# Optimization experiments

Measured on AMD Instinct MI355X. Metric: run time of the kernel, lower is better.

Reference implementation:

```python
import jax, jax.numpy as jnp
import numpy as np

# model constants (match init_kwargs)
B, T, D = 2, 2048, 2048          # batch, seq_len, d_model (= d_in = d_out)
H, G = 32, 8                     # num_heads, num_kv_groups
HD = D // H                      # head_dim = 64
GROUP = H // G                   # 4 query heads per KV group
ROPE_BASE = 10000.0


def _apply_rope(x):
    # x: (b, heads, t, hd); rotate-half RoPE over absolute positions 0..t-1
    t = x.shape[2]
    half = HD // 2
    inv_freq = 1.0 / (ROPE_BASE ** (jnp.arange(half, dtype=jnp.float32) * 2.0 / HD))
    ang = jnp.arange(t, dtype=jnp.float32)[:, None] * inv_freq[None, :]   # (t, half)
    cos, sin = jnp.cos(ang), jnp.sin(ang)
    x1, x2 = x[..., :half], x[..., half:]
    out = jnp.concatenate([x1 * cos - x2 * sin, x2 * cos + x1 * sin], axis=-1)
    return out.astype(x.dtype)


def setup_inputs() -> dict:
    key = jax.random.key(0)
    kx, kq, kk, kv, ko = jax.random.split(key, 5)
    scale = 0.02
    x = jax.random.normal(kx, (B, T, D), dtype=jnp.float32)
    # linear weights stored as (in, out) so y = x @ W
    Wq = jax.random.normal(kq, (D, D), dtype=jnp.float32) * scale
    Wk = jax.random.normal(kk, (D, G * HD), dtype=jnp.float32) * scale
    Wv = jax.random.normal(kv, (D, G * HD), dtype=jnp.float32) * scale
    Wo = jax.random.normal(ko, (D, D), dtype=jnp.float32) * scale
    return {"x": x, "Wq": Wq, "Wk": Wk, "Wv": Wv, "Wo": Wo}


def reference(x, Wq, Wk, Wv, Wo):
    b, t, _ = x.shape
    q = (x @ Wq).reshape(b, t, H, HD).transpose(0, 2, 1, 3)   # (b, H, t, hd)
    k = (x @ Wk).reshape(b, t, G, HD).transpose(0, 2, 1, 3)   # (b, G, t, hd)
    v = (x @ Wv).reshape(b, t, G, HD).transpose(0, 2, 1, 3)
    q = _apply_rope(q)
    k = _apply_rope(k)
    # GQA: physically duplicate K/V per query-head group (repeat_interleave)
    k = jnp.repeat(k, GROUP, axis=1)                          # (b, H, t, hd)
    v = jnp.repeat(v, GROUP, axis=1)
    scores = jnp.einsum('bhqd,bhkd->bhqk', q, k)              # (b, H, t, t)
    causal = jnp.triu(jnp.ones((t, t), dtype=bool), k=1)
    scores = jnp.where(causal, -jnp.inf, scores)
    attn = jax.nn.softmax(scores / jnp.sqrt(jnp.float32(HD)), axis=-1)
    ctx = jnp.einsum('bhqk,bhkd->bhqd', attn, v)              # (b, H, t, hd)
    # faithful to source: transpose(-2, -1) then reshape (NOT the usual (b,t,H,hd) order)
    ctx = jnp.swapaxes(ctx, -2, -1).reshape(b, t, D)
    return ctx @ Wo
```

## Files before the change

kernel.cpp:

```cpp
#include <hip/hip_runtime.h>

typedef unsigned short u16;
typedef unsigned int u32;
typedef __bf16 bf16x8 __attribute__((ext_vector_type(8)));
typedef float f32x4 __attribute__((ext_vector_type(4)));
typedef u16 u16x8 __attribute__((ext_vector_type(8)));
typedef __attribute__((address_space(1))) const void gvoid;
typedef __attribute__((address_space(3))) void svoid;

#define T_SEQ 2048
#define NEG_INF (-__builtin_huge_valf())

__device__ __forceinline__ u16 f2bf(float f) {
  union { float f; unsigned u; } x; x.f = f;
  unsigned u = x.u;
  return (u16)((u + 0x7FFFu + ((u >> 16) & 1u)) >> 16);
}
__device__ __forceinline__ float bf2f(u16 h) {
  union { unsigned u; float f; } x; x.u = ((unsigned)h) << 16;
  return x.f;
}
__device__ __forceinline__ u32 pack_bf2(float lo, float hi) {
  u32 r;
  asm("v_cvt_pk_bf16_f32 %0, %1, %2" : "=v"(r) : "v"(lo), "v"(hi));
  return r;
}
__device__ __forceinline__ int swz16(int row, int col16) {
  int blk = (col16 >> 3) ^ (row & 7) ^ ((row >> 3) & 7);
  return row * 64 + ((blk & 7) << 3) + (col16 & 7);
}

__global__ __launch_bounds__(256) void cast_f32_bf16(const float* __restrict__ in,
                                                     u16* __restrict__ out, long n) {
  long i = ((long)blockIdx.x * 256 + threadIdx.x) * 4;
  if (i >= n) return;
  float4 v = *(const float4*)(in + i);
  ushort4 o;
  o.x = f2bf(v.x); o.y = f2bf(v.y); o.z = f2bf(v.z); o.w = f2bf(v.w);
  *(ushort4*)(out + i) = o;
}

__global__ __launch_bounds__(256) void transpose_cast(const float* __restrict__ W,
                                                      u16* __restrict__ WT, int K, int N) {
  __shared__ float tile[32][33];
  int nb = blockIdx.x * 32, kb = blockIdx.y * 32;
  int tx = threadIdx.x, ty = threadIdx.y;
  #pragma unroll
  for (int i = 0; i < 32; i += 8)
    tile[ty + i][tx] = W[(size_t)(kb + ty + i) * N + nb + tx];
  __syncthreads();
  #pragma unroll
  for (int i = 0; i < 32; i += 8)
    WT[(size_t)(nb + ty + i) * K + kb + tx] = f2bf(tile[tx][ty + i]);
}

__global__ __launch_bounds__(256) void rope_table_k(float2* __restrict__ tab) {
  int idx = blockIdx.x * 256 + threadIdx.x;
  int t = idx >> 5, d = idx & 31;
  float inv = powf(10000.0f, -(float)d / 32.0f);
  float ang = (float)t * inv;
  float s, c;
  sincosf(ang, &s, &c);
  tab[idx] = make_float2(c, s);
}

template<int MODE>
__global__ __launch_bounds__(256) void gemm_bt(const u16* __restrict__ A,
                                               const u16* __restrict__ BT,
                                               void* __restrict__ Cout,
                                               int M, int N, int K,
                                               const float2* __restrict__ tab) {
  __shared__ __align__(16) u16 As[128 * 64];
  __shared__ __align__(16) u16 Bs[128 * 64];
  const int tid = threadIdx.x;
  const int w = tid >> 6, lane = tid & 63;
  const int r16 = lane & 15, kg = lane >> 4;
  const size_t rowBase = (size_t)blockIdx.y * 128;
  const size_t colBase = (size_t)blockIdx.x * 128;
  const int wm = (w >> 1) * 64, wn = (w & 1) * 64;
  f32x4 acc[4][4] = {};

  const u16* Abase = A + (rowBase + w * 32 + (lane >> 3)) * (size_t)K + (lane & 7) * 8;
  const u16* Bbase = BT + (colBase + w * 32 + (lane >> 3)) * (size_t)K + (lane & 7) * 8;

  for (int k0 = 0; k0 < K; k0 += 64) {
    __syncthreads();
    #pragma unroll
    for (int i = 0; i < 4; ++i) {
      __builtin_amdgcn_global_load_lds((gvoid*)(Abase + (size_t)i * 8 * K + k0),
                                       (svoid*)(&As[(w * 32 + i * 8) * 64]), 16, 0, 0);
      __builtin_amdgcn_global_load_lds((gvoid*)(Bbase + (size_t)i * 8 * K + k0),
                                       (svoid*)(&Bs[(w * 32 + i * 8) * 64]), 16, 0, 0);
    }
    __syncthreads();
    #pragma unroll
    for (int kk = 0; kk < 2; ++kk) {
      bf16x8 af[4], bfv[4];
      #pragma unroll
      for (int mi = 0; mi < 4; ++mi)
        af[mi] = *(const bf16x8*)(&As[(wm + mi * 16 + r16) * 64 + kk * 32 + kg * 8]);
      #pragma unroll
      for (int ni = 0; ni < 4; ++ni)
        bfv[ni] = *(const bf16x8*)(&Bs[(wn + ni * 16 + r16) * 64 + kk * 32 + kg * 8]);
      __builtin_amdgcn_s_setprio(1);
      #pragma unroll
      for (int mi = 0; mi < 4; ++mi)
        #pragma unroll
        for (int ni = 0; ni < 4; ++ni)
          acc[mi][ni] = __builtin_amdgcn_mfma_f32_16x16x32_bf16(af[mi], bfv[ni], acc[mi][ni], 0, 0, 0);
      __builtin_amdgcn_s_setprio(0);
    }
  }

  if (MODE == 2 && colBase < 2560) {
    #pragma unroll
    for (int mi = 0; mi < 4; ++mi)
      #pragma unroll
      for (int p = 0; p < 2; ++p) {
        int d = (wn + p * 16 + r16) & 63;
        #pragma unroll
        for (int r = 0; r < 4; ++r) {
          int t = (int)((rowBase + wm + mi * 16 + kg * 4 + r) & (T_SEQ - 1));
          float2 cs = tab[t * 32 + d];
          float x1 = acc[mi][p][r], x2 = acc[mi][p + 2][r];
          acc[mi][p][r]     = x1 * cs.x - x2 * cs.y;
          acc[mi][p + 2][r] = x2 * cs.x + x1 * cs.y;
        }
      }
  }

  #pragma unroll
  for (int mi = 0; mi < 4; ++mi)
    #pragma unroll
    for (int ni = 0; ni < 4; ++ni) {
      size_t row = rowBase + wm + mi * 16 + kg * 4;
      size_t col = colBase + wn + ni * 16 + r16;
      if (MODE == 1) {
        float* C = (float*)Cout;
        #pragma unroll
        for (int r = 0; r < 4; ++r) C[(row + r) * N + col] = acc[mi][ni][r];
      } else {
        u16* C = (u16*)Cout;
        #pragma unroll
        for (int r = 0; r < 4; ++r) C[(row + r) * N + col] = f2bf(acc[mi][ni][r]);
      }
    }
}

__global__ __launch_bounds__(256) void attn_fwd(const u16* __restrict__ QKV,
                                                u16* __restrict__ ctxT) {
  const int bh = blockIdx.x, pr = blockIdx.y;
  const int b = bh >> 5, h = bh & 31, g = h >> 2;
  const int tid = threadIdx.x, w = tid >> 6, lane = tid & 63;
  const int r16 = lane & 15, kg = lane >> 4;
  const int LD = 3072;

  const u16* Qp = QKV + (size_t)b * T_SEQ * LD + h * 64;
  const u16* Kp = QKV + (size_t)b * T_SEQ * LD + 2048 + g * 64;
  const u16* Vp = QKV + (size_t)b * T_SEQ * LD + 2560 + g * 64;

  __shared__ __align__(16) u16 Kt[2][64 * 64];
  __shared__ __align__(16) u16 Vt[2][64 * 64];

  const float SCALE = 0.18033688f;
  const int srow = tid >> 3, sc8 = tid & 7;
  const int klr = (lane >> 3);
  const int kblk = lane & 7;

  for (int hf = 0; hf < 2; ++hf) {
    const int qt = hf ? (15 - pr) : pr;
    const int qbase = qt * 128, wq = qbase + w * 32;

    bf16x8 qf[2][2];
    #pragma unroll
    for (int mi = 0; mi < 2; ++mi)
      #pragma unroll
      for (int ks = 0; ks < 2; ++ks)
        qf[mi][ks] = *(const bf16x8*)(Qp + (size_t)(wq + mi * 16 + r16) * LD + ks * 32 + kg * 8);

    f32x4 acc[4][2] = {};
    float m_i[2] = {NEG_INF, NEG_INF}, l_i[2] = {0.0f, 0.0f};
    const int nkt = (qbase + 128) >> 6;

    {
      #pragma unroll
      for (int i = 0; i < 2; ++i) {
        int lr = w * 16 + i * 8 + klr;
        int sb = kblk ^ ((lr & 7) ^ ((lr >> 3) & 7));
        __builtin_amdgcn_global_load_lds((gvoid*)(Kp + (size_t)lr * LD + sb * 8),
                                         (svoid*)(&Kt[0][(w * 16 + i * 8) * 64]), 16, 0, 0);
      }
      bf16x8 v0 = *(const bf16x8*)(Vp + (size_t)(2 * srow) * LD + sc8 * 8);
      bf16x8 v1 = *(const bf16x8*)(Vp + (size_t)(2 * srow + 1) * LD + sc8 * 8);
      const u16* va = (const u16*)&v0;
      const u16* vb = (const u16*)&v1;
      #pragma unroll
      for (int j = 0; j < 8; ++j)
        *(u32*)(&Vt[0][swz16(sc8 * 8 + j, 2 * srow)]) = (u32)va[j] | ((u32)vb[j] << 16);
      __syncthreads();
    }

    for (int kt = 0; kt < nkt; ++kt) {
      const int kvb = kt << 6;
      const int cur = kt & 1;
      const bool st = (kt + 1 < nkt);
      bf16x8 v0, v1;
      if (st) {
        #pragma unroll
        for (int i = 0; i < 2; ++i) {
          int lr = w * 16 + i * 8 + klr;
          int sb = kblk ^ ((lr & 7) ^ ((lr >> 3) & 7));
          __builtin_amdgcn_global_load_lds((gvoid*)(Kp + (size_t)(kvb + 64 + lr) * LD + sb * 8),
                                           (svoid*)(&Kt[cur ^ 1][(w * 16 + i * 8) * 64]), 16, 0, 0);
        }
        v0 = *(const bf16x8*)(Vp + (size_t)(kvb + 64 + 2 * srow) * LD + sc8 * 8);
        v1 = *(const bf16x8*)(Vp + (size_t)(kvb + 64 + 2 * srow + 1) * LD + sc8 * 8);
      }

      if (kvb <= wq + 31) {
        f32x4 stv[4][2] = {};
        #pragma unroll
        for (int ks = 0; ks < 2; ++ks) {
          bf16x8 kf[4];
          #pragma unroll
          for (int ni = 0; ni < 4; ++ni)
            kf[ni] = *(const bf16x8*)(&Kt[cur][swz16(ni * 16 + r16, ks * 32 + kg * 8)]);
          __builtin_amdgcn_s_setprio(1);
          #pragma unroll
          for (int ni = 0; ni < 4; ++ni)
            #pragma unroll
            for (int mi = 0; mi < 2; ++mi)
              stv[ni][mi] = __builtin_amdgcn_mfma_f32_16x16x32_bf16(kf[ni], qf[mi][ks], stv[ni][mi], 0, 0, 0);
          __builtin_amdgcn_s_setprio(0);
        }

        if (kvb + 63 > wq) {
          #pragma unroll
          for (int mi = 0; mi < 2; ++mi) {
            const int q = wq + mi * 16 + r16;
            #pragma unroll
            for (int ni = 0; ni < 4; ++ni)
              #pragma unroll
              for (int r = 0; r < 4; ++r) {
                int kv = kvb + ni * 16 + kg * 4 + r;
                if (kv > q) stv[ni][mi][r] = NEG_INF;
              }
          }
        }

        float tmx[2];
        #pragma unroll
        for (int mi = 0; mi < 2; ++mi) {
          float pm = NEG_INF;
          #pragma unroll
          for (int ni = 0; ni < 4; ++ni)
            #pragma unroll
            for (int r = 0; r < 4; ++r) pm = fmaxf(pm, stv[ni][mi][r]);
          pm = fmaxf(pm, __shfl_xor(pm, 16, 64));
          pm = fmaxf(pm, __shfl_xor(pm, 32, 64));
          tmx[mi] = pm;
        }
        bool upd = ((tmx[0] - m_i[0]) * SCALE > 8.0f) || ((tmx[1] - m_i[1]) * SCALE > 8.0f);
        if (__any(upd)) {
          #pragma unroll
          for (int mi = 0; mi < 2; ++mi) {
            float mnew = fmaxf(m_i[mi], tmx[mi]);
            float alpha = exp2f((m_i[mi] - mnew) * SCALE);
            m_i[mi] = mnew;
            l_i[mi] *= alpha;
            #pragma unroll
            for (int di = 0; di < 4; ++di)
              #pragma unroll
              for (int r = 0; r < 4; ++r) acc[di][mi][r] *= alpha;
          }
        }

        u32 pkk[2][4][2];
        #pragma unroll
        for (int mi = 0; mi < 2; ++mi) {
          float nm = m_i[mi] * SCALE;
          float rs = 0.0f;
          #pragma unroll
          for (int ni = 0; ni < 4; ++ni) {
            float p0 = exp2f(fmaf(stv[ni][mi][0], SCALE, -nm));
            float p1 = exp2f(fmaf(stv[ni][mi][1], SCALE, -nm));
            float p2 = exp2f(fmaf(stv[ni][mi][2], SCALE, -nm));
            float p3 = exp2f(fmaf(stv[ni][mi][3], SCALE, -nm));
            rs += (p0 + p1) + (p2 + p3);
            pkk[mi][ni][0] = pack_bf2(p0, p1);
            pkk[mi][ni][1] = pack_bf2(p2, p3);
          }
          rs += __shfl_xor(rs, 16, 64);
          rs += __shfl_xor(rs, 32, 64);
          l_i[mi] += rs;
        }

        #pragma unroll
        for (int ks = 0; ks < 2; ++ks) {
          bf16x8 vfr[4];
          #pragma unroll
          for (int di = 0; di < 4; ++di)
            vfr[di] = *(const bf16x8*)(&Vt[cur][swz16(di * 16 + r16, ks * 32 + kg * 8)]);
          const int s0 = (kg & 1) * 32 + r16;
          const int s1 = s0 + 16;
          const bool hi = (kg >> 1) != 0;
          #pragma unroll
          for (int mi = 0; mi < 2; ++mi) {
            u32 a0 = __shfl(pkk[mi][2 * ks][0], s0, 64);
            u32 b0 = __shfl(pkk[mi][2 * ks + 1][0], s0, 64);
            u32 a1 = __shfl(pkk[mi][2 * ks][1], s0, 64);
            u32 b1 = __shfl(pkk[mi][2 * ks + 1][1], s0, 64);
            u32 a2 = __shfl(pkk[mi][2 * ks][0], s1, 64);
            u32 b2 = __shfl(pkk[mi][2 * ks + 1][0], s1, 64);
            u32 a3 = __shfl(pkk[mi][2 * ks][1], s1, 64);
            u32 b3 = __shfl(pkk[mi][2 * ks + 1][1], s1, 64);
            union { u32 u[4]; bf16x8 v; } pu;
            pu.u[0] = hi ? b0 : a0;
            pu.u[1] = hi ? b1 : a1;
            pu.u[2] = hi ? b2 : a2;
            pu.u[3] = hi ? b3 : a3;
            __builtin_amdgcn_s_setprio(1);
            #pragma unroll
            for (int di = 0; di < 4; ++di)
              acc[di][mi] = __builtin_amdgcn_mfma_f32_16x16x32_bf16(vfr[di], pu.v, acc[di][mi], 0, 0, 0);
            __builtin_amdgcn_s_setprio(0);
          }
        }
      }

      if (st) {
        const u16* va = (const u16*)&v0;
        const u16* vb = (const u16*)&v1;
        #pragma unroll
        for (int j = 0; j < 8; ++j)
          *(u32*)(&Vt[cur ^ 1][swz16(sc8 * 8 + j, 2 * srow)]) = (u32)va[j] | ((u32)vb[j] << 16);
      }
      __syncthreads();
    }

    float inv[2] = {1.0f / l_i[0], 1.0f / l_i[1]};
    #pragma unroll
    for (int di = 0; di < 4; ++di)
      #pragma unroll
      for (int mi = 0; mi < 2; ++mi)
        #pragma unroll
        for (int r = 0; r < 4; ++r) {
          size_t row = (size_t)(b * 2048 + h * 64 + di * 16 + kg * 4 + r);
          ctxT[row * 2048 + wq + mi * 16 + r16] = f2bf(acc[di][mi][r] * inv[mi]);
        }
  }
}

extern "C" void kernel_launch(void* const* d_in, const int* in_sizes, int n_in,
                              void* d_out, int out_size, void* d_ws, size_t ws_size,
                              hipStream_t stream) {
  const float* x  = (const float*)d_in[0];
  const float* Wq = (const float*)d_in[1];
  const float* Wk = (const float*)d_in[2];
  const float* Wv = (const float*)d_in[3];
  const float* Wo = (const float*)d_in[4];
  float* out = (float*)d_out;
  char* ws = (char*)d_ws;

  u16* xb     = (u16*)(ws);
  u16* QKVb   = (u16*)(ws + 16777216);
  u16* ctxT   = (u16*)(ws + 41943040);
  u16* WqkvT  = (u16*)(ws + 58720256);
  u16* WoT    = (u16*)(ws + 71303168);
  float2* tab = (float2*)(ws + 79691776);

  cast_f32_bf16<<<8192, 256, 0, stream>>>(x, xb, 8388608L);
  rope_table_k<<<256, 256, 0, stream>>>(tab);
  transpose_cast<<<dim3(64, 64), dim3(32, 8), 0, stream>>>(Wq, WqkvT, 2048, 2048);
  transpose_cast<<<dim3(16, 64), dim3(32, 8), 0, stream>>>(Wk, WqkvT + 2048L * 2048, 2048, 512);
  transpose_cast<<<dim3(16, 64), dim3(32, 8), 0, stream>>>(Wv, WqkvT + 2560L * 2048, 2048, 512);
  transpose_cast<<<dim3(64, 64), dim3(32, 8), 0, stream>>>(Wo, WoT, 2048, 2048);

  gemm_bt<2><<<dim3(24, 32), 256, 0, stream>>>(xb, WqkvT, QKVb, 4096, 3072, 2048, tab);

  attn_fwd<<<dim3(64, 8), 256, 0, stream>>>(QKVb, ctxT);

  gemm_bt<1><<<dim3(16, 32), 256, 0, stream>>>(ctxT, WoT, out, 4096, 2048, 2048, nullptr);
}
```

Measured before the change: 434.8 us.

## Split attention work across eight waves with 16 query rows each

```diff
diff --git a/kernel.cpp b/kernel.cpp
--- a/kernel.cpp
+++ b/kernel.cpp
@@ -4,7 +4,7 @@
 typedef unsigned int u32;
 typedef __bf16 bf16x8 __attribute__((ext_vector_type(8)));
 typedef float f32x4 __attribute__((ext_vector_type(4)));
-typedef u16 u16x8 __attribute__((ext_vector_type(8)));
+typedef u16 u16x4 __attribute__((ext_vector_type(4)));
 typedef __attribute__((address_space(1))) const void gvoid;
 typedef __attribute__((address_space(3))) void svoid;
 
@@ -15,10 +15,6 @@
   union { float f; unsigned u; } x; x.f = f;
   unsigned u = x.u;
   return (u16)((u + 0x7FFFu + ((u >> 16) & 1u)) >> 16);
-}
-__device__ __forceinline__ float bf2f(u16 h) {
-  union { unsigned u; float f; } x; x.u = ((unsigned)h) << 16;
-  return x.f;
 }
 __device__ __forceinline__ u32 pack_bf2(float lo, float hi) {
   u32 r;
@@ -147,8 +143,8 @@
     }
 }
 
-__global__ __launch_bounds__(256) void attn_fwd(const u16* __restrict__ QKV,
-                                                u16* __restrict__ ctxT) {
+__global__ __launch_bounds__(512, 4) void attn_fwd(const u16* __restrict__ QKV,
+                                                   u16* __restrict__ ctxT) {
   const int bh = blockIdx.x, pr = blockIdx.y;
   const int b = bh >> 5, h = bh & 31, g = h >> 2;
   const int tid = threadIdx.x, w = tid >> 6, lane = tid & 63;
@@ -163,40 +159,31 @@
   __shared__ __align__(16) u16 Vt[2][64 * 64];
 
   const float SCALE = 0.18033688f;
-  const int srow = tid >> 3, sc8 = tid & 7;
-  const int klr = (lane >> 3);
-  const int kblk = lane & 7;
+  const int srow = tid >> 4, sc4 = tid & 15;
+  const int klr = w * 8 + (lane >> 3);
+  const int ksb = (lane & 7) ^ (klr & 7) ^ ((klr >> 3) & 7);
 
   for (int hf = 0; hf < 2; ++hf) {
     const int qt = hf ? (15 - pr) : pr;
-    const int qbase = qt * 128, wq = qbase + w * 32;
-
-    bf16x8 qf[2][2];
-    #pragma unroll
-    for (int mi = 0; mi < 2; ++mi)
-      #pragma unroll
-      for (int ks = 0; ks < 2; ++ks)
-        qf[mi][ks] = *(const bf16x8*)(Qp + (size_t)(wq + mi * 16 + r16) * LD + ks * 32 + kg * 8);
-
-    f32x4 acc[4][2] = {};
-    float m_i[2] = {NEG_INF, NEG_INF}, l_i[2] = {0.0f, 0.0f};
-    const int nkt = (qbase + 128) >> 6;
+    const int qbase = qt * 128, wq = qbase + w * 16;
+    const int nkt = 2 * qt + 2;
+
+    bf16x8 qf[2];
+    #pragma unroll
+    for (int ks = 0; ks < 2; ++ks)
+      qf[ks] = *(const bf16x8*)(Qp + (size_t)(wq + r16) * LD + ks * 32 + kg * 8);
+
+    f32x4 acc[4] = {};
+    float m_i = NEG_INF, l_i = 0.0f;
 
     {
-      #pragma unroll
-      for (int i = 0; i < 2; ++i) {
-        int lr = w * 16 + i * 8 + klr;
-        int sb = kblk ^ ((lr & 7) ^ ((lr >> 3) & 7));
-        __builtin_amdgcn_global_load_lds((gvoid*)(Kp + (size_t)lr * LD + sb * 8),
-                                         (svoid*)(&Kt[0][(w * 16 + i * 8) * 64]), 16, 0, 0);
-      }
-      bf16x8 v0 = *(const bf16x8*)(Vp + (size_t)(2 * srow) * LD + sc8 * 8);
-      bf16x8 v1 = *(const bf16x8*)(Vp + (size_t)(2 * srow + 1) * LD + sc8 * 8);
-      const u16* va = (const u16*)&v0;
-      const u16* vb = (const u16*)&v1;
-      #pragma unroll
-      for (int j = 0; j < 8; ++j)
-        *(u32*)(&Vt[0][swz16(sc8 * 8 + j, 2 * srow)]) = (u32)va[j] | ((u32)vb[j] << 16);
+      __builtin_amdgcn_global_load_lds((gvoid*)(Kp + (size_t)klr * LD + ksb * 8),
+                                       (svoid*)(&Kt[0][w * 512]), 16, 0, 0);
+      u16x4 a0 = *(const u16x4*)(Vp + (size_t)(2 * srow) * LD + sc4 * 4);
+      u16x4 a1 = *(const u16x4*)(Vp + (size_t)(2 * srow + 1) * LD + sc4 * 4);
+      #pragma unroll
+      for (int j = 0; j < 4; ++j)
+        *(u32*)(&Vt[0][swz16(sc4 * 4 + j, 2 * srow)]) = (u32)a0[j] | ((u32)a1[j] << 16);
       __syncthreads();
     }
 
@@ -204,21 +191,16 @@
       const int kvb = kt << 6;
       const int cur = kt & 1;
       const bool st = (kt + 1 < nkt);
-      bf16x8 v0, v1;
+      u16x4 a0, a1;
       if (st) {
-        #pragma unroll
-        for (int i = 0; i < 2; ++i) {
-          int lr = w * 16 + i * 8 + klr;
-          int sb = kblk ^ ((lr & 7) ^ ((lr >> 3) & 7));
-          __builtin_amdgcn_global_load_lds((gvoid*)(Kp + (size_t)(kvb + 64 + lr) * LD + sb * 8),
-                                           (svoid*)(&Kt[cur ^ 1][(w * 16 + i * 8) * 64]), 16, 0, 0);
-        }
-        v0 = *(const bf16x8*)(Vp + (size_t)(kvb + 64 + 2 * srow) * LD + sc8 * 8);
-        v1 = *(const bf16x8*)(Vp + (size_t)(kvb + 64 + 2 * srow + 1) * LD + sc8 * 8);
-      }
-
-      if (kvb <= wq + 31) {
-        f32x4 stv[4][2] = {};
+        __builtin_amdgcn_global_load_lds((gvoid*)(Kp + (size_t)(kvb + 64 + klr) * LD + ksb * 8),
+                                         (svoid*)(&Kt[cur ^ 1][w * 512]), 16, 0, 0);
+        a0 = *(const u16x4*)(Vp + (size_t)(kvb + 64 + 2 * srow) * LD + sc4 * 4);
+        a1 = *(const u16x4*)(Vp + (size_t)(kvb + 64 + 2 * srow + 1) * LD + sc4 * 4);
+      }
+
+      if (kvb <= wq + 15) {
+        f32x4 stv[4] = {};
         #pragma unroll
         for (int ks = 0; ks < 2; ++ks) {
           bf16x8 kf[4];
@@ -228,72 +210,53 @@
           __builtin_amdgcn_s_setprio(1);
           #pragma unroll
           for (int ni = 0; ni < 4; ++ni)
-            #pragma unroll
-            for (int mi = 0; mi < 2; ++mi)
-              stv[ni][mi] = __builtin_amdgcn_mfma_f32_16x16x32_bf16(kf[ni], qf[mi][ks], stv[ni][mi], 0, 0, 0);
+            stv[ni] = __builtin_amdgcn_mfma_f32_16x16x32_bf16(kf[ni], qf[ks], stv[ni], 0, 0, 0);
           __builtin_amdgcn_s_setprio(0);
         }
 
         if (kvb + 63 > wq) {
-          #pragma unroll
-          for (int mi = 0; mi < 2; ++mi) {
-            const int q = wq + mi * 16 + r16;
-            #pragma unroll
-            for (int ni = 0; ni < 4; ++ni)
-              #pragma unroll
-              for (int r = 0; r < 4; ++r) {
-                int kv = kvb + ni * 16 + kg * 4 + r;
-                if (kv > q) stv[ni][mi][r] = NEG_INF;
-              }
-          }
-        }
-
-        float tmx[2];
-        #pragma unroll
-        for (int mi = 0; mi < 2; ++mi) {
-          float pm = NEG_INF;
+          const int q = wq + r16;
           #pragma unroll
           for (int ni = 0; ni < 4; ++ni)
             #pragma unroll
-            for (int r = 0; r < 4; ++r) pm = fmaxf(pm, stv[ni][mi][r]);
-          pm = fmaxf(pm, __shfl_xor(pm, 16, 64));
-          pm = fmaxf(pm, __shfl_xor(pm, 32, 64));
-          tmx[mi] = pm;
-        }
-        bool upd = ((tmx[0] - m_i[0]) * SCALE > 8.0f) || ((tmx[1] - m_i[1]) * SCALE > 8.0f);
-        if (__any(upd)) {
-          #pragma unroll
-          for (int mi = 0; mi < 2; ++mi) {
-            float mnew = fmaxf(m_i[mi], tmx[mi]);
-            float alpha = exp2f((m_i[mi] - mnew) * SCALE);
-            m_i[mi] = mnew;
-            l_i[mi] *= alpha;
+            for (int r = 0; r < 4; ++r)
+              if (kvb + ni * 16 + kg * 4 + r > q) stv[ni][r] = NEG_INF;
+        }
+
+        float pm = NEG_INF;
+        #pragma unroll
+        for (int ni = 0; ni < 4; ++ni)
+          #pragma unroll
+          for (int r = 0; r < 4; ++r) pm = fmaxf(pm, stv[ni][r]);
+        pm = fmaxf(pm, __shfl_xor(pm, 16, 64));
+        pm = fmaxf(pm, __shfl_xor(pm, 32, 64));
+        if (__any((pm - m_i) * SCALE > 8.0f)) {
+          float mnew = fmaxf(m_i, pm);
+          float alpha = exp2f((m_i - mnew) * SCALE);
+          m_i = mnew;
+          l_i *= alpha;
+          #pragma unroll
+          for (int di = 0; di < 4; ++di)
             #pragma unroll
-            for (int di = 0; di < 4; ++di)
-              #pragma unroll
-              for (int r = 0; r < 4; ++r) acc[di][mi][r] *= alpha;
-          }
-        }
-
-        u32 pkk[2][4][2];
-        #pragma unroll
-        for (int mi = 0; mi < 2; ++mi) {
-          float nm = m_i[mi] * SCALE;
-          float rs = 0.0f;
-          #pragma unroll
-          for (int ni = 0; ni < 4; ++ni) {
-            float p0 = exp2f(fmaf(stv[ni][mi][0], SCALE, -nm));
-            float p1 = exp2f(fmaf(stv[ni][mi][1], SCALE, -nm));
-            float p2 = exp2f(fmaf(stv[ni][mi][2], SCALE, -nm));
-            float p3 = exp2f(fmaf(stv[ni][mi][3], SCALE, -nm));
-            rs += (p0 + p1) + (p2 + p3);
-            pkk[mi][ni][0] = pack_bf2(p0, p1);
-            pkk[mi][ni][1] = pack_bf2(p2, p3);
-          }
-          rs += __shfl_xor(rs, 16, 64);
-          rs += __shfl_xor(rs, 32, 64);
-          l_i[mi] += rs;
-        }
+            for (int r = 0; r < 4; ++r) acc[di][r] *= alpha;
+        }
+
+        u32 pkk[4][2];
+        float nm = m_i * SCALE;
+        float rs = 0.0f;
+        #pragma unroll
+        for (int ni = 0; ni < 4; ++ni) {
+          float p0 = exp2f(fmaf(stv[ni][0], SCALE, -nm));
+          float p1 = exp2f(fmaf(stv[ni][1], SCALE, -nm));
+          float p2 = exp2f(fmaf(stv[ni][2], SCALE, -nm));
+          float p3 = exp2f(fmaf(stv[ni][3], SCALE, -nm));
+          rs += (p0 + p1) + (p2 + p3);
+          pkk[ni][0] = pack_bf2(p0, p1);
+          pkk[ni][1] = pack_bf2(p2, p3);
+        }
+        rs += __shfl_xor(rs, 16, 64);
+        rs += __shfl_xor(rs, 32, 64);
+        l_i += rs;
 
         #pragma unroll
         for (int ks = 0; ks < 2; ++ks) {
@@ -304,50 +267,43 @@
           const int s0 = (kg & 1) * 32 + r16;
           const int s1 = s0 + 16;
           const bool hi = (kg >> 1) != 0;
-          #pragma unroll
-          for (int mi = 0; mi < 2; ++mi) {
-            u32 a0 = __shfl(pkk[mi][2 * ks][0], s0, 64);
-            u32 b0 = __shfl(pkk[mi][2 * ks + 1][0], s0, 64);
-            u32 a1 = __shfl(pkk[mi][2 * ks][1], s0, 64);
-            u32 b1 = __shfl(pkk[mi][2 * ks + 1][1], s0, 64);
-            u32 a2 = __shfl(pkk[mi][2 * ks][0], s1, 64);
-            u32 b2 = __shfl(pkk[mi][2 * ks + 1][0], s1, 64);
-            u32 a3 = __shfl(pkk[mi][2 * ks][1], s1, 64);
-            u32 b3 = __shfl(pkk[mi][2 * ks + 1][1], s1, 64);
-            union { u32 u[4]; bf16x8 v; } pu;
-            pu.u[0] = hi ? b0 : a0;
-            pu.u[1] = hi ? b1 : a1;
-            pu.u[2] = hi ? b2 : a2;
-            pu.u[3] = hi ? b3 : a3;
-            __builtin_amdgcn_s_setprio(1);
-            #pragma unroll
-            for (int di = 0; di < 4; ++di)
-              acc[di][mi] = __builtin_amdgcn_mfma_f32_16x16x32_bf16(vfr[di], pu.v, acc[di][mi], 0, 0, 0);
-            __builtin_amdgcn_s_setprio(0);
-          }
+          u32 c0 = __shfl(pkk[2 * ks][0], s0, 64);
+          u32 d0 = __shfl(pkk[2 * ks + 1][0], s0, 64);
+          u32 c1 = __shfl(pkk[2 * ks][1], s0, 64);
+          u32 d1 = __shfl(pkk[2 * ks + 1][1], s0, 64);
+          u32 c2 = __shfl(pkk[2 * ks][0], s1, 64);
+          u32 d2 = __shfl(pkk[2 * ks + 1][0], s1, 64);
+          u32 c3 = __shfl(pkk[2 * ks][1], s1, 64);
+          u32 d3 = __shfl(pkk[2 * ks + 1][1], s1, 64);
+          union { u32 u[4]; bf16x8 v; } pu;
+          pu.u[0] = hi ? d0 : c0;
+          pu.u[1] = hi ? d1 : c1;
+          pu.u[2] = hi ? d2 : c2;
+          pu.u[3] = hi ? d3 : c3;
+          __builtin_amdgcn_s_setprio(1);
+          #pragma unroll
+          for (int di = 0; di < 4; ++di)
+            acc[di] = __builtin_amdgcn_mfma_f32_16x16x32_bf16(vfr[di], pu.v, acc[di], 0, 0, 0);
+          __builtin_amdgcn_s_setprio(0);
         }
       }
 
       if (st) {
-        const u16* va = (const u16*)&v0;
-        const u16* vb = (const u16*)&v1;
-        #pragma unroll
-        for (int j = 0; j < 8; ++j)
-          *(u32*)(&Vt[cur ^ 1][swz16(sc8 * 8 + j, 2 * srow)]) = (u32)va[j] | ((u32)vb[j] << 16);
+        #pragma unroll
+        for (int j = 0; j < 4; ++j)
+          *(u32*)(&Vt[cur ^ 1][swz16(sc4 * 4 + j, 2 * srow)]) = (u32)a0[j] | ((u32)a1[j] << 16);
       }
       __syncthreads();
     }
 
-    float inv[2] = {1.0f / l_i[0], 1.0f / l_i[1]};
+    float inv = 1.0f / l_i;
     #pragma unroll
     for (int di = 0; di < 4; ++di)
       #pragma unroll
-      for (int mi = 0; mi < 2; ++mi)
-        #pragma unroll
-        for (int r = 0; r < 4; ++r) {
-          size_t row = (size_t)(b * 2048 + h * 64 + di * 16 + kg * 4 + r);
-          ctxT[row * 2048 + wq + mi * 16 + r16] = f2bf(acc[di][mi][r] * inv[mi]);
-        }
+      for (int r = 0; r < 4; ++r) {
+        size_t row = (size_t)(b * 2048 + h * 64 + di * 16 + kg * 4 + r);
+        ctxT[row * 2048 + wq + r16] = f2bf(acc[di][r] * inv);
+      }
   }
 }
 
@@ -378,7 +334,7 @@
 
   gemm_bt<2><<<dim3(24, 32), 256, 0, stream>>>(xb, WqkvT, QKVb, 4096, 3072, 2048, tab);
 
-  attn_fwd<<<dim3(64, 8), 256, 0, stream>>>(QKVb, ctxT);
+  attn_fwd<<<dim3(64, 8), 512, 0, stream>>>(QKVb, ctxT);
 
   gemm_bt<1><<<dim3(16, 32), 256, 0, stream>>>(ctxT, WoT, out, 4096, 2048, 2048, nullptr);
 }
```

New measurement: 395.3 us. 9.1% less time.
